# Kernel optimization log

Hardware: AMD Instinct MI355X
Metric: run time of the kernel (lower is better)

Reference implementation:

```python
import jax, jax.numpy as jnp
import numpy as np

G = 512        # graphs in batch
N_PER = 256    # nodes per graph (equal-size graphs)
D = 128        # embed_dim
E_PER = 4096   # edges per graph
KEEP = 0.5
K = int(np.ceil(KEEP * N_PER))  # 128 nodes kept per graph (PyG topk: ceil(ratio*n))
N = G * N_PER
E = G * E_PER


def setup_inputs() -> dict:
    key = jax.random.key(0)
    k1, k2, k3, k4, k5 = jax.random.split(key, 5)
    x = jax.random.normal(k1, (N, D), jnp.float32)
    offs = (jnp.arange(G, dtype=jnp.int32) * N_PER)[:, None]
    src = jax.random.randint(k2, (G, E_PER), 0, N_PER, dtype=jnp.int32) + offs
    dst = jax.random.randint(k3, (G, E_PER), 0, N_PER, dtype=jnp.int32) + offs
    edge_index = jnp.stack([src.reshape(-1), dst.reshape(-1)], axis=0)  # [2, E], within-graph edges
    graph_indicator = jnp.repeat(jnp.arange(G, dtype=jnp.int32), N_PER)  # [N]
    gcn_w = jax.random.normal(k4, (D, 1), jnp.float32) / np.sqrt(D)
    gcn_b = jnp.zeros((1,), jnp.float32)
    lin_w = jax.random.normal(k5, (2 * D, D), jnp.float32) / np.sqrt(2 * D)
    lin_b = jnp.zeros((D,), jnp.float32)
    return {"input_feature": x, "graph_indicator": graph_indicator, "edge_index": edge_index,
            "gcn_w": gcn_w, "gcn_b": gcn_b, "lin_w": lin_w, "lin_b": lin_b}


def gcn_conv(x, edge_index, w, b):
    # PyG GCNConv: add self-loops, symmetric normalization, aggregate at target (edge_index[1]).
    n = x.shape[0]
    loop = jnp.arange(n, dtype=edge_index.dtype)
    row = jnp.concatenate([edge_index[0], loop])  # source
    col = jnp.concatenate([edge_index[1], loop])  # target
    deg = jax.ops.segment_sum(jnp.ones_like(col, dtype=x.dtype), col, num_segments=n)
    dinv = jax.lax.rsqrt(deg)  # deg >= 1 due to self-loops
    norm = dinv[row] * dinv[col]            # [E+N]
    xw = x @ w                              # [N, out]
    msg = xw[row] * norm[:, None]           # gather + scale
    agg = jax.ops.segment_sum(msg, col, num_segments=n)
    return agg + b


def reference(input_feature, graph_indicator, edge_index, gcn_w, gcn_b, lin_w, lin_b):
    # SAGPool: attention scores via GCNConv(d -> 1)
    score = gcn_conv(input_feature, edge_index, gcn_w, gcn_b).squeeze(-1)  # [N]
    # per-graph top-k mask (equal-size graphs -> reshape)
    s = score.reshape(G, N_PER)
    _, idx = jax.lax.top_k(s, K)                                          # [G, K]
    mask = jnp.zeros((G, N_PER), bool).at[jnp.arange(G)[:, None], idx].set(True)
    # gated features of kept nodes: x[mask] * tanh(score[mask])
    feat = (input_feature * jnp.tanh(score)[:, None]).reshape(G, N_PER, D)
    m = mask[..., None]
    # global mean/max pool over kept nodes per graph (exactly K kept per graph)
    mean = jnp.sum(jnp.where(m, feat, 0.0), axis=1) / K                   # [G, D]
    mx = jnp.max(jnp.where(m, feat, -jnp.inf), axis=1)                    # [G, D]
    readout = jnp.concatenate([mean, mx], axis=1)                         # [G, 2D]
    return readout @ lin_w + lin_b                                        # [G, D]
```

## Files before the change

### kernel.cpp

```cpp
#include <hip/hip_runtime.h>
#include <math.h>

#define NG   512
#define NPER 256
#define DD   128
#define EPER 4096
#define KK   128
#define NT   1024
#define NW   16

#define SFX_SCALE 4194304.0f
#define SFX_INV   2.384185791015625e-07f

__global__ __launch_bounds__(NT, 8) void sag_fused(
    const float* __restrict__ x,
    const int*   __restrict__ esrc,
    const int*   __restrict__ edst,
    const float* __restrict__ gcn_w,
    const float* __restrict__ gcn_b,
    const float* __restrict__ lin_w,
    const float* __restrict__ lin_b,
    float* __restrict__ out)
{
  const int g    = blockIdx.x;
  const int tid  = threadIdx.x;
  const int lane = tid & 63;
  const int wave = tid >> 6;
  const int j    = lane & 15;
  const int sub  = lane >> 4;
  const int slot = wave * 4 + sub;

  __shared__ int    sDeg[NPER];
  __shared__ int    sRank[NPER];
  __shared__ int    sXWi[NPER];
  __shared__ __align__(16) int   sFx[NPER];
  __shared__ float  sXW[NPER];
  __shared__ float  sDinv[NPER];
  __shared__ __align__(16) float sScore[NPER];
  __shared__ float2 sGF[NPER];
  __shared__ float  sPoolS[NW][DD];
  __shared__ float  sPoolM[NW][DD];
  __shared__ float2 sR2[DD];
  float* sR = (float*)sR2;

  const int4* es4 = (const int4*)(esrc + (size_t)g * EPER);
  const int4* ed4 = (const int4*)(edst + (size_t)g * EPER);
  int4 sa = es4[tid];
  int4 da = ed4[tid];

  const float4* xg4 = (const float4*)(x + (size_t)g * NPER * DD);
  const int colbase = slot * 32 + j;
  float4 q0[4], q1[4];
  #pragma unroll
  for (int r = 0; r < 4; ++r) {
    q0[r] = xg4[r * 2048 + colbase];
    q1[r] = xg4[r * 2048 + colbase + 16];
  }
  float4 wa = ((const float4*)gcn_w)[j];
  float4 wb = ((const float4*)gcn_w)[16 + j];

  if (tid < NPER) { sDeg[tid] = 1; sRank[tid] = 0; }
  __syncthreads();

  atomicAdd(&sDeg[da.x & 255], 1);
  atomicAdd(&sDeg[da.y & 255], 1);
  atomicAdd(&sDeg[da.z & 255], 1);
  atomicAdd(&sDeg[da.w & 255], 1);

  #pragma unroll
  for (int r = 0; r < 4; ++r) {
    float acc = q0[r].x*wa.x + q0[r].y*wa.y + q0[r].z*wa.z + q0[r].w*wa.w
              + q1[r].x*wb.x + q1[r].y*wb.y + q1[r].z*wb.z + q1[r].w*wb.w;
    acc += __shfl_xor(acc, 1);
    acc += __shfl_xor(acc, 2);
    acc += __shfl_xor(acc, 4);
    acc += __shfl_xor(acc, 8);
    if (j == 0) sXW[r * 64 + slot] = acc;
  }
  __syncthreads();

  if (tid < NPER) {
    float dv = 1.0f / sqrtf((float)sDeg[tid]);
    int   xi = __float2int_rn(sXW[tid] * dv * SFX_SCALE);
    sDinv[tid] = dv;
    sXWi[tid]  = xi;
    sFx[tid]   = xi;
  }
  __syncthreads();

  {
    int v0 = sXWi[sa.x & 255];
    int v1 = sXWi[sa.y & 255];
    int v2 = sXWi[sa.z & 255];
    int v3 = sXWi[sa.w & 255];
    atomicAdd(&sFx[da.x & 255], v0);
    atomicAdd(&sFx[da.y & 255], v1);
    atomicAdd(&sFx[da.z & 255], v2);
    atomicAdd(&sFx[da.w & 255], v3);
  }
  __syncthreads();

  if (tid < NPER) sScore[tid] = sDinv[tid] * ((float)sFx[tid] * SFX_INV);
  __syncthreads();

  {
    const float4* sScore4 = (const float4*)sScore;
    int node = tid & 255;
    int seg  = tid >> 8;
    float s_i = sScore[node];
    int base = seg * 16;
    int part = 0;
    #pragma unroll 8
    for (int t = 0; t < 16; ++t) {
      float4 v = sScore4[base + t];
      int jj = (base + t) * 4;
      part += (v.x > s_i) || (v.x == s_i && (jj + 0) < node);
      part += (v.y > s_i) || (v.y == s_i && (jj + 1) < node);
      part += (v.z > s_i) || (v.z == s_i && (jj + 2) < node);
      part += (v.w > s_i) || (v.w == s_i && (jj + 3) < node);
    }
    atomicAdd(&sRank[node], part);
  }
  __syncthreads();

  if (tid < NPER) {
    bool kp = sRank[tid] < KK;
    float gate = tanhf(sScore[tid] + gcn_b[0]);
    sGF[tid] = make_float2(kp ? gate : 0.0f, kp ? 0.0f : INFINITY);
  }
  __syncthreads();

  float su0=0,su1=0,su2=0,su3=0,su4=0,su5=0,su6=0,su7=0;
  float mx0=-INFINITY,mx1=-INFINITY,mx2=-INFINITY,mx3=-INFINITY;
  float mx4=-INFINITY,mx5=-INFINITY,mx6=-INFINITY,mx7=-INFINITY;
  #pragma unroll
  for (int r = 0; r < 4; ++r) {
    float2 gf = sGF[r * 64 + slot];
    float g1 = gf.x, fb = gf.y;
    float a;
    a = q0[r].x * g1; su0 += a; mx0 = fmaxf(mx0, a - fb);
    a = q0[r].y * g1; su1 += a; mx1 = fmaxf(mx1, a - fb);
    a = q0[r].z * g1; su2 += a; mx2 = fmaxf(mx2, a - fb);
    a = q0[r].w * g1; su3 += a; mx3 = fmaxf(mx3, a - fb);
    a = q1[r].x * g1; su4 += a; mx4 = fmaxf(mx4, a - fb);
    a = q1[r].y * g1; su5 += a; mx5 = fmaxf(mx5, a - fb);
    a = q1[r].z * g1; su6 += a; mx6 = fmaxf(mx6, a - fb);
    a = q1[r].w * g1; su7 += a; mx7 = fmaxf(mx7, a - fb);
  }
  #define RED_S(v) v += __shfl_xor(v,16); v += __shfl_xor(v,32);
  #define RED_M(v) v = fmaxf(v,__shfl_xor(v,16)); v = fmaxf(v,__shfl_xor(v,32));
  RED_S(su0) RED_S(su1) RED_S(su2) RED_S(su3)
  RED_S(su4) RED_S(su5) RED_S(su6) RED_S(su7)
  RED_M(mx0) RED_M(mx1) RED_M(mx2) RED_M(mx3)
  RED_M(mx4) RED_M(mx5) RED_M(mx6) RED_M(mx7)
  if (sub == 0) {
    ((float4*)&sPoolS[wave][4 * j])[0]      = make_float4(su0, su1, su2, su3);
    ((float4*)&sPoolS[wave][64 + 4 * j])[0] = make_float4(su4, su5, su6, su7);
    ((float4*)&sPoolM[wave][4 * j])[0]      = make_float4(mx0, mx1, mx2, mx3);
    ((float4*)&sPoolM[wave][64 + 4 * j])[0] = make_float4(mx4, mx5, mx6, mx7);
  }
  __syncthreads();

  if (tid < DD) {
    float s = 0.f;
    #pragma unroll
    for (int w = 0; w < NW; ++w) s += sPoolS[w][tid];
    sR[tid] = s * (1.0f / KK);
  } else if (tid < 2 * DD) {
    int d = tid - DD;
    float m = -INFINITY;
    #pragma unroll
    for (int w = 0; w < NW; ++w) m = fmaxf(m, sPoolM[w][d]);
    sR[tid] = m;
  }
  __syncthreads();

  const float2* lw2 = (const float2*)lin_w;
  float a0 = 0.f, a1 = 0.f;
  #pragma unroll
  for (int t = 0; t < 8; ++t) {
    int k2 = wave * 8 + t;
    float2 rv = sR2[k2];
    float2 p0 = lw2[(2 * k2) * 64 + lane];
    float2 p1 = lw2[(2 * k2 + 1) * 64 + lane];
    a0 += rv.x * p0.x + rv.y * p1.x;
    a1 += rv.x * p0.y + rv.y * p1.y;
  }
  float2* sP2 = (float2*)sPoolS;
  sP2[wave * 64 + lane] = make_float2(a0, a1);
  __syncthreads();
  if (wave == 0) {
    float2 a = sP2[lane];
    #pragma unroll
    for (int w = 1; w < NW; ++w) { float2 p = sP2[w * 64 + lane]; a.x += p.x; a.y += p.y; }
    float2 bb = ((const float2*)lin_b)[lane];
    a.x += bb.x; a.y += bb.y;
    ((float2*)out)[(size_t)g * 64 + lane] = a;
  }
}

extern "C" void kernel_launch(void* const* d_in, const int* in_sizes, int n_in,
                              void* d_out, int out_size, void* d_ws, size_t ws_size,
                              hipStream_t stream) {
  const float* x  = (const float*)d_in[0];
  const int*   ei = (const int*)d_in[2];
  const float* gw = (const float*)d_in[3];
  const float* gb = (const float*)d_in[4];
  const float* lw = (const float*)d_in[5];
  const float* lb = (const float*)d_in[6];
  float* out = (float*)d_out;
  const int E = in_sizes[2] / 2;
  sag_fused<<<NG, NT, 0, stream>>>(x, ei, ei + E, gw, gb, lw, lb, out);
}
```

Before: 119.2 us.

## Split fused SAGPool kernel into score and pooling kernels with smaller blocks

The single 1024-thread fused kernel becomes two kernels. A 256-thread scoring kernel computes degrees, GCN scores, ranks and gates, and writes per-node gate/mask pairs to a global buffer. A 512-thread pooling kernel then re-reads x to do the masked mean/max pooling and the final linear layer. The rank counting now runs one thread per node over all 256 scores, which removes the rank atomics. The split is meant to raise occupancy and shorten barrier-heavy phases, but it reads x from HBM twice (about 64 MB each pass) and adds a launch and a global round trip.

```diff
diff --git a/kernel.cpp b/kernel.cpp
--- a/kernel.cpp
+++ b/kernel.cpp
@@ -6,18 +6,118 @@
 #define DD   128
 #define EPER 4096
 #define KK   128
-#define NT   1024
-#define NW   16
 
 #define SFX_SCALE 4194304.0f
 #define SFX_INV   2.384185791015625e-07f
 
-__global__ __launch_bounds__(NT, 8) void sag_fused(
+__device__ float2 g_gf[NG * NPER];
+
+__global__ __launch_bounds__(256, 5) void sag_score(
     const float* __restrict__ x,
     const int*   __restrict__ esrc,
     const int*   __restrict__ edst,
     const float* __restrict__ gcn_w,
-    const float* __restrict__ gcn_b,
+    const float* __restrict__ gcn_b)
+{
+  const int g    = blockIdx.x;
+  const int tid  = threadIdx.x;
+  const int lane = tid & 63;
+  const int wave = tid >> 6;
+  const int j    = lane & 15;
+  const int sub  = lane >> 4;
+  const int slot = wave * 4 + sub;
+
+  __shared__ int    sDeg[NPER];
+  __shared__ int    sXWi[NPER];
+  __shared__ __align__(16) int   sFx[NPER];
+  __shared__ float  sXW[NPER];
+  __shared__ float  sDinv[NPER];
+  __shared__ __align__(16) float sScore[NPER];
+
+  const int4* es4 = (const int4*)(esrc + (size_t)g * EPER);
+  const int4* ed4 = (const int4*)(edst + (size_t)g * EPER);
+  int4 sa[4], da[4];
+  #pragma unroll
+  for (int k = 0; k < 4; ++k) { da[k] = ed4[k * 256 + tid]; sa[k] = es4[k * 256 + tid]; }
+
+  float4 wa = ((const float4*)gcn_w)[j];
+  float4 wb = ((const float4*)gcn_w)[16 + j];
+
+  sDeg[tid] = 1;
+  __syncthreads();
+
+  #pragma unroll
+  for (int k = 0; k < 4; ++k) {
+    atomicAdd(&sDeg[da[k].x & 255], 1);
+    atomicAdd(&sDeg[da[k].y & 255], 1);
+    atomicAdd(&sDeg[da[k].z & 255], 1);
+    atomicAdd(&sDeg[da[k].w & 255], 1);
+  }
+
+  const float4* xg4 = (const float4*)(x + (size_t)g * NPER * DD);
+  #pragma unroll 4
+  for (int r = 0; r < 16; ++r) {
+    const int node = r * 16 + slot;
+    float4 a4 = xg4[node * 32 + j];
+    float4 b4 = xg4[node * 32 + 16 + j];
+    float acc = a4.x*wa.x + a4.y*wa.y + a4.z*wa.z + a4.w*wa.w
+              + b4.x*wb.x + b4.y*wb.y + b4.z*wb.z + b4.w*wb.w;
+    acc += __shfl_xor(acc, 1);
+    acc += __shfl_xor(acc, 2);
+    acc += __shfl_xor(acc, 4);
+    acc += __shfl_xor(acc, 8);
+    if (j == 0) sXW[node] = acc;
+  }
+  __syncthreads();
+
+  {
+    float dv = 1.0f / sqrtf((float)sDeg[tid]);
+    int   xi = __float2int_rn(sXW[tid] * dv * SFX_SCALE);
+    sDinv[tid] = dv;
+    sXWi[tid]  = xi;
+    sFx[tid]   = xi;
+  }
+  __syncthreads();
+
+  #pragma unroll
+  for (int k = 0; k < 4; ++k) {
+    int v0 = sXWi[sa[k].x & 255];
+    int v1 = sXWi[sa[k].y & 255];
+    int v2 = sXWi[sa[k].z & 255];
+    int v3 = sXWi[sa[k].w & 255];
+    atomicAdd(&sFx[da[k].x & 255], v0);
+    atomicAdd(&sFx[da[k].y & 255], v1);
+    atomicAdd(&sFx[da[k].z & 255], v2);
+    atomicAdd(&sFx[da[k].w & 255], v3);
+  }
+  __syncthreads();
+
+  sScore[tid] = sDinv[tid] * ((float)sFx[tid] * SFX_INV);
+  __syncthreads();
+
+  {
+    const float4* sScore4 = (const float4*)sScore;
+    float s_i = sScore[tid];
+    int part = 0;
+    #pragma unroll 8
+    for (int t = 0; t < 64; ++t) {
+      float4 v = sScore4[t];
+      int jj = t * 4;
+      part += (v.x > s_i) || (v.x == s_i && (jj + 0) < tid);
+      part += (v.y > s_i) || (v.y == s_i && (jj + 1) < tid);
+      part += (v.z > s_i) || (v.z == s_i && (jj + 2) < tid);
+      part += (v.w > s_i) || (v.w == s_i && (jj + 3) < tid);
+    }
+    bool kp = part < KK;
+    float gate = tanhf(s_i + gcn_b[0]);
+    g_gf[(size_t)g * NPER + tid] = make_float2(kp ? gate : 0.0f, kp ? 0.0f : INFINITY);
+  }
+}
+
+#define NTB 512
+#define NWB 8
+__global__ __launch_bounds__(NTB, 4) void sag_pool(
+    const float* __restrict__ x,
     const float* __restrict__ lin_w,
     const float* __restrict__ lin_b,
     float* __restrict__ out)
@@ -30,112 +130,29 @@
   const int sub  = lane >> 4;
   const int slot = wave * 4 + sub;
 
-  __shared__ int    sDeg[NPER];
-  __shared__ int    sRank[NPER];
-  __shared__ int    sXWi[NPER];
-  __shared__ __align__(16) int   sFx[NPER];
-  __shared__ float  sXW[NPER];
-  __shared__ float  sDinv[NPER];
-  __shared__ __align__(16) float sScore[NPER];
   __shared__ float2 sGF[NPER];
-  __shared__ float  sPoolS[NW][DD];
-  __shared__ float  sPoolM[NW][DD];
+  __shared__ float  sPoolS[NWB][DD];
+  __shared__ float  sPoolM[NWB][DD];
   __shared__ float2 sR2[DD];
   float* sR = (float*)sR2;
 
-  const int4* es4 = (const int4*)(esrc + (size_t)g * EPER);
-  const int4* ed4 = (const int4*)(edst + (size_t)g * EPER);
-  int4 sa = es4[tid];
-  int4 da = ed4[tid];
-
   const float4* xg4 = (const float4*)(x + (size_t)g * NPER * DD);
   const int colbase = slot * 32 + j;
-  float4 q0[4], q1[4];
-  #pragma unroll
-  for (int r = 0; r < 4; ++r) {
-    q0[r] = xg4[r * 2048 + colbase];
-    q1[r] = xg4[r * 2048 + colbase + 16];
-  }
-  float4 wa = ((const float4*)gcn_w)[j];
-  float4 wb = ((const float4*)gcn_w)[16 + j];
-
-  if (tid < NPER) { sDeg[tid] = 1; sRank[tid] = 0; }
-  __syncthreads();
-
-  atomicAdd(&sDeg[da.x & 255], 1);
-  atomicAdd(&sDeg[da.y & 255], 1);
-  atomicAdd(&sDeg[da.z & 255], 1);
-  atomicAdd(&sDeg[da.w & 255], 1);
-
-  #pragma unroll
-  for (int r = 0; r < 4; ++r) {
-    float acc = q0[r].x*wa.x + q0[r].y*wa.y + q0[r].z*wa.z + q0[r].w*wa.w
-              + q1[r].x*wb.x + q1[r].y*wb.y + q1[r].z*wb.z + q1[r].w*wb.w;
-    acc += __shfl_xor(acc, 1);
-    acc += __shfl_xor(acc, 2);
-    acc += __shfl_xor(acc, 4);
-    acc += __shfl_xor(acc, 8);
-    if (j == 0) sXW[r * 64 + slot] = acc;
-  }
-  __syncthreads();
-
-  if (tid < NPER) {
-    float dv = 1.0f / sqrtf((float)sDeg[tid]);
-    int   xi = __float2int_rn(sXW[tid] * dv * SFX_SCALE);
-    sDinv[tid] = dv;
-    sXWi[tid]  = xi;
-    sFx[tid]   = xi;
-  }
-  __syncthreads();
-
-  {
-    int v0 = sXWi[sa.x & 255];
-    int v1 = sXWi[sa.y & 255];
-    int v2 = sXWi[sa.z & 255];
-    int v3 = sXWi[sa.w & 255];
-    atomicAdd(&sFx[da.x & 255], v0);
-    atomicAdd(&sFx[da.y & 255], v1);
-    atomicAdd(&sFx[da.z & 255], v2);
-    atomicAdd(&sFx[da.w & 255], v3);
-  }
-  __syncthreads();
-
-  if (tid < NPER) sScore[tid] = sDinv[tid] * ((float)sFx[tid] * SFX_INV);
-  __syncthreads();
-
-  {
-    const float4* sScore4 = (const float4*)sScore;
-    int node = tid & 255;
-    int seg  = tid >> 8;
-    float s_i = sScore[node];
-    int base = seg * 16;
-    int part = 0;
-    #pragma unroll 8
-    for (int t = 0; t < 16; ++t) {
-      float4 v = sScore4[base + t];
-      int jj = (base + t) * 4;
-      part += (v.x > s_i) || (v.x == s_i && (jj + 0) < node);
-      part += (v.y > s_i) || (v.y == s_i && (jj + 1) < node);
-      part += (v.z > s_i) || (v.z == s_i && (jj + 2) < node);
-      part += (v.w > s_i) || (v.w == s_i && (jj + 3) < node);
-    }
-    atomicAdd(&sRank[node], part);
-  }
-  __syncthreads();
-
-  if (tid < NPER) {
-    bool kp = sRank[tid] < KK;
-    float gate = tanhf(sScore[tid] + gcn_b[0]);
-    sGF[tid] = make_float2(kp ? gate : 0.0f, kp ? 0.0f : INFINITY);
-  }
+  float4 q0[8], q1[8];
+  #pragma unroll
+  for (int r = 0; r < 8; ++r) {
+    q0[r] = xg4[r * 1024 + colbase];
+    q1[r] = xg4[r * 1024 + colbase + 16];
+  }
+  if (tid < NPER) sGF[tid] = g_gf[(size_t)g * NPER + tid];
   __syncthreads();
 
   float su0=0,su1=0,su2=0,su3=0,su4=0,su5=0,su6=0,su7=0;
   float mx0=-INFINITY,mx1=-INFINITY,mx2=-INFINITY,mx3=-INFINITY;
   float mx4=-INFINITY,mx5=-INFINITY,mx6=-INFINITY,mx7=-INFINITY;
   #pragma unroll
-  for (int r = 0; r < 4; ++r) {
-    float2 gf = sGF[r * 64 + slot];
+  for (int r = 0; r < 8; ++r) {
+    float2 gf = sGF[r * 32 + slot];
     float g1 = gf.x, fb = gf.y;
     float a;
     a = q0[r].x * g1; su0 += a; mx0 = fmaxf(mx0, a - fb);
@@ -164,13 +181,13 @@
   if (tid < DD) {
     float s = 0.f;
     #pragma unroll
-    for (int w = 0; w < NW; ++w) s += sPoolS[w][tid];
+    for (int w = 0; w < NWB; ++w) s += sPoolS[w][tid];
     sR[tid] = s * (1.0f / KK);
   } else if (tid < 2 * DD) {
     int d = tid - DD;
     float m = -INFINITY;
     #pragma unroll
-    for (int w = 0; w < NW; ++w) m = fmaxf(m, sPoolM[w][d]);
+    for (int w = 0; w < NWB; ++w) m = fmaxf(m, sPoolM[w][d]);
     sR[tid] = m;
   }
   __syncthreads();
@@ -178,8 +195,8 @@
   const float2* lw2 = (const float2*)lin_w;
   float a0 = 0.f, a1 = 0.f;
   #pragma unroll
-  for (int t = 0; t < 8; ++t) {
-    int k2 = wave * 8 + t;
+  for (int t = 0; t < 16; ++t) {
+    int k2 = wave * 16 + t;
     float2 rv = sR2[k2];
     float2 p0 = lw2[(2 * k2) * 64 + lane];
     float2 p1 = lw2[(2 * k2 + 1) * 64 + lane];
@@ -192,7 +209,7 @@
   if (wave == 0) {
     float2 a = sP2[lane];
     #pragma unroll
-    for (int w = 1; w < NW; ++w) { float2 p = sP2[w * 64 + lane]; a.x += p.x; a.y += p.y; }
+    for (int w = 1; w < NWB; ++w) { float2 p = sP2[w * 64 + lane]; a.x += p.x; a.y += p.y; }
     float2 bb = ((const float2*)lin_b)[lane];
     a.x += bb.x; a.y += bb.y;
     ((float2*)out)[(size_t)g * 64 + lane] = a;
@@ -210,5 +227,6 @@
   const float* lb = (const float*)d_in[6];
   float* out = (float*)d_out;
   const int E = in_sizes[2] / 2;
-  sag_fused<<<NG, NT, 0, stream>>>(x, ei, ei + E, gw, gb, lw, lb, out);
+  sag_score<<<NG, 256, 0, stream>>>(x, ei, ei + E, gw, gb);
+  sag_pool <<<NG, NTB, 0, stream>>>(x, lw, lb, out);
 }
```

Measured after the change: 138.4 us. +16.1%, slower.
